# Kernel tuning notes

Measured on AMD Instinct MI355X. Metric: run time of the kernel, lower is better.

## Reference

```python
import jax, jax.numpy as jnp
import numpy as np

BATCH, IN_DIM, HID, OUT_DIM, Z = 8192, 2048, 4096, 2048, 4
CONN_P = 0.5  # Bernoulli keep-probability y


def random_activation(h, ids):
    # ids: [dim] int32 in [0,5); per-channel nonlinearity applied over batch.
    ids = ids[None, :]
    return jnp.select(
        [ids == 0, ids == 1, ids == 2, ids == 3],
        [jax.nn.relu(h), jax.nn.sigmoid(h), jnp.tanh(h), jnp.where(h >= 0, h, 0.1 * h)],
        jax.nn.selu(h),
    )


def _make_linear(key, fan_in, fan_out):
    kw, kb, km = jax.random.split(key, 3)
    w = jax.random.normal(kw, (fan_out, fan_in), dtype=jnp.float32)
    mask = jax.random.bernoulli(km, CONN_P, (fan_out, fan_in)).astype(jnp.float32)
    b = jax.random.normal(kb, (fan_out,), dtype=jnp.float32)
    return w * mask, b


def setup_inputs() -> dict:
    key = jax.random.key(0)
    ks = jax.random.split(key, 16)
    inp = {"input_pattern": jax.random.normal(ks[0], (BATCH, IN_DIM), dtype=jnp.float32)}
    dims = [(IN_DIM, HID)] + [(HID, HID)] * Z + [(HID, OUT_DIM)]  # z+2 Linear layers
    for i, (fi, fo) in enumerate(dims):
        w, b = _make_linear(ks[1 + i], fi, fo)
        inp[f"w{i}"] = w
        inp[f"b{i}"] = b
        inp[f"ids{i}"] = jax.random.randint(ks[8 + i], (fo,), 0, 5, dtype=jnp.int32)
    return inp


def reference(input_pattern, w0, b0, ids0, w1, b1, ids1, w2, b2, ids2,
              w3, b3, ids3, w4, b4, ids4, w5, b5, ids5):
    ws = (w0, w1, w2, w3, w4, w5)
    bs = (b0, b1, b2, b3, b4, b5)
    ids = (ids0, ids1, ids2, ids3, ids4, ids5)
    h = input_pattern
    for w, b, i in zip(ws, bs, ids):
        h = random_activation(h @ w.T + b, i)
    return h
```

## Files before the change

### kernel.cpp

```cpp
#include <hip/hip_runtime.h>

typedef _Float16 f16;
typedef _Float16 f16x8 __attribute__((ext_vector_type(8)));
typedef float f32x4 __attribute__((ext_vector_type(4)));

__device__ __forceinline__ void gload_lds16(const void* g, void* l) {
  __builtin_amdgcn_global_load_lds(
      (const __attribute__((address_space(1))) void*)g,
      (__attribute__((address_space(3))) void*)l, 16, 0, 0);
}

__device__ __forceinline__ float act_apply(float x, int id) {
  switch (id) {
    case 0: return fmaxf(x, 0.0f);
    case 1: return 1.0f / (1.0f + __expf(-x));
    case 2: return tanhf(x);
    case 3: return x >= 0.0f ? x : 0.1f * x;
    default: return 1.0507009873554805f *
                    (x > 0.0f ? x : 1.6732632423543772f * expm1f(x));
  }
}

__global__ __launch_bounds__(256, 3)
void gemm128w(const f16* __restrict__ A, const f16* __restrict__ W,
              const float* __restrict__ bias, const int* __restrict__ ids,
              float Sa, float invSn, f16* __restrict__ outp,
              int M, int N, int K) {
  __shared__ f16 LB[16384];
  const int tid  = (int)threadIdx.x;
  const int lane = tid & 63;
  const int wid  = tid >> 6;
  const int wr   = (wid >> 1) * 64;
  const int wc   = (wid & 1) * 64;

  const int nbc = N >> 7;
  const int b   = (int)blockIdx.x;
  const int x   = b & 7;
  const int r   = b >> 3;
  int brow, bcol;
  if (nbc >= 32) {
    brow = ((x >> 1) * 16 + (r & 15)) << 7;
    bcol = ((x & 1) * (nbc >> 1) + (r >> 4)) << 7;
  } else {
    brow = (x * 8 + (r & 7)) << 7;
    bcol = (r >> 3) << 7;
  }

  const int d0 = tid << 4;
  const int d1 = d0 + 4096;
  const int s0 = d0 ^ (((d0 >> 7) & 7) << 4);
  const int s1 = d1 ^ (((d1 >> 7) & 7) << 4);
  const int r0 = s0 >> 6, c0 = (s0 >> 4) & 3;
  const int r1 = s1 >> 6, c1 = (s1 >> 4) & 3;

  const f16* pA0 = A + (long)(brow + r0) * K + c0 * 8;
  const f16* pA1 = A + (long)(brow + r1) * K + c1 * 8;
  const int e0 = tid << 3;
  const int e1 = e0 + 2048;

  const int fr = lane & 15;
  const int kb = lane >> 4;
  const int xorv = ((fr >> 1) & 7) << 4;
  int offA[4];
#pragma unroll
  for (int m = 0; m < 4; ++m)
    offA[m] = (((wr + m * 16 + fr) << 6) + (kb << 4)) ^ xorv;

  const f16* pw[4];
#pragma unroll
  for (int n = 0; n < 4; ++n)
    pw[n] = W + (long)(bcol + wc + n * 16 + fr) * K + kb * 8;

  f32x4 acc[4][4];
#pragma unroll
  for (int m = 0; m < 4; ++m)
#pragma unroll
    for (int n = 0; n < 4; ++n) acc[m][n] = (f32x4){0.f, 0.f, 0.f, 0.f};

  const int nt = K >> 5;

  gload_lds16(pA0, &LB[e0]);
  gload_lds16(pA1, &LB[e1]);
  f16x8 w0[4], w1[4], af[4];
#pragma unroll
  for (int n = 0; n < 4; ++n) w0[n] = *(const f16x8*)(pw[n]);
  __syncthreads();

  for (int t = 0; t < nt; t += 2) {
    {
      const long kk = (long)(t + 1) << 5;
      gload_lds16(pA0 + kk, &LB[4096 + e0]);
      gload_lds16(pA1 + kk, &LB[4096 + e1]);
#pragma unroll
      for (int n = 0; n < 4; ++n) w1[n] = *(const f16x8*)(pw[n] + kk);
      const char* bA = (const char*)&LB[0];
#pragma unroll
      for (int m = 0; m < 4; ++m) af[m] = *(const f16x8*)(bA + offA[m]);
#pragma unroll
      for (int m = 0; m < 4; ++m)
#pragma unroll
        for (int n = 0; n < 4; ++n)
          acc[m][n] = __builtin_amdgcn_mfma_f32_16x16x32_f16(af[m], w0[n],
                                                             acc[m][n], 0, 0, 0);
      __syncthreads();
    }
    {
      if (t + 2 < nt) {
        const long kk = (long)(t + 2) << 5;
        gload_lds16(pA0 + kk, &LB[e0]);
        gload_lds16(pA1 + kk, &LB[e1]);
#pragma unroll
        for (int n = 0; n < 4; ++n) w0[n] = *(const f16x8*)(pw[n] + kk);
      }
      const char* bA = (const char*)&LB[0] + 8192;
#pragma unroll
      for (int m = 0; m < 4; ++m) af[m] = *(const f16x8*)(bA + offA[m]);
#pragma unroll
      for (int m = 0; m < 4; ++m)
#pragma unroll
        for (int n = 0; n < 4; ++n)
          acc[m][n] = __builtin_amdgcn_mfma_f32_16x16x32_f16(af[m], w1[n],
                                                             acc[m][n], 0, 0, 0);
      if (t + 2 < nt) __syncthreads();
    }
  }

  __syncthreads();
  char* eb = (char*)&LB[0] + wid * 8192;
  const int r4 = (lane >> 4) << 2;
#pragma unroll
  for (int n = 0; n < 4; ++n) {
    const int gcol = bcol + wc + n * 16 + fr;
    const float bv = bias[gcol];
    const int id   = ids[gcol];
#pragma unroll
    for (int m = 0; m < 4; ++m)
#pragma unroll
      for (int i = 0; i < 4; ++i) {
        const float y = act_apply(acc[m][n][i] * Sa + bv, id);
        const int w = ((m * 16 + r4 + i) * 64 + n * 16 + fr) * 2;
        *(f16*)(eb + (w ^ (((w >> 7) & 7) << 4))) = (f16)(y * invSn);
      }
  }
  __syncthreads();
#pragma unroll
  for (int j = 0; j < 8; ++j) {
    const int lrow = j * 8 + (lane >> 3);
    const int rd = lrow * 128 + (lane & 7) * 16;
    const f16x8 v = *(const f16x8*)(eb + (rd ^ (((rd >> 7) & 7) << 4)));
    *(f16x8*)&outp[(long)(brow + wr + lrow) * N + bcol + wc + (lane & 7) * 8] = v;
  }
}

template <bool FINAL>
__global__ __launch_bounds__(256, 4)
void gemm128(const f16* __restrict__ A, const f16* __restrict__ W,
             const float* __restrict__ bias, const int* __restrict__ ids,
             float Sa, float invSn, void* __restrict__ outv,
             int M, int N, int K) {
  __shared__ f16 lA[2][128 * 32];
  __shared__ f16 lB[2][128 * 32];

  const int tid  = (int)threadIdx.x;
  const int lane = tid & 63;
  const int wid  = tid >> 6;
  const int wr   = (wid >> 1) * 64;
  const int wc   = (wid & 1) * 64;

  const int nbc = N >> 7;
  const int b   = (int)blockIdx.x;
  const int x   = b & 7;
  const int r   = b >> 3;
  int brow, bcol;
  if (nbc >= 32) {
    brow = ((x >> 1) * 16 + (r & 15)) << 7;
    bcol = ((x & 1) * (nbc >> 1) + (r >> 4)) << 7;
  } else {
    brow = (x * 8 + (r & 7)) << 7;
    bcol = (r >> 3) << 7;
  }

  const int d0 = tid << 4;
  const int d1 = d0 + 4096;
  const int s0 = d0 ^ (((d0 >> 7) & 7) << 4);
  const int s1 = d1 ^ (((d1 >> 7) & 7) << 4);
  const int r0 = s0 >> 6, c0 = (s0 >> 4) & 3;
  const int r1 = s1 >> 6, c1 = (s1 >> 4) & 3;

  const f16* pA0 = A + (long)(brow + r0) * K + c0 * 8;
  const f16* pA1 = A + (long)(brow + r1) * K + c1 * 8;
  const f16* pB0 = W + (long)(bcol + r0) * K + c0 * 8;
  const f16* pB1 = W + (long)(bcol + r1) * K + c1 * 8;
  const int e0 = tid << 3;
  const int e1 = e0 + 2048;

  const int fr = lane & 15;
  const int kb = lane >> 4;
  const int xorv = ((fr >> 1) & 7) << 4;

  int offA[4], offB[4];
#pragma unroll
  for (int m = 0; m < 4; ++m)
    offA[m] = (((wr + m * 16 + fr) << 6) + (kb << 4)) ^ xorv;
#pragma unroll
  for (int n = 0; n < 4; ++n)
    offB[n] = (((wc + n * 16 + fr) << 6) + (kb << 4)) ^ xorv;

  f32x4 acc[4][4];
#pragma unroll
  for (int m = 0; m < 4; ++m)
#pragma unroll
    for (int n = 0; n < 4; ++n) acc[m][n] = (f32x4){0.f, 0.f, 0.f, 0.f};

  const int nt = K >> 5;
  int buf = 0;

  gload_lds16(pA0, &lA[0][e0]);
  gload_lds16(pA1, &lA[0][e1]);
  gload_lds16(pB0, &lB[0][e0]);
  gload_lds16(pB1, &lB[0][e1]);
  __syncthreads();

  for (int t = 0; t < nt; ++t) {
    if (t + 1 < nt) {
      const long kk = (long)(t + 1) << 5;
      gload_lds16(pA0 + kk, &lA[buf ^ 1][e0]);
      gload_lds16(pA1 + kk, &lA[buf ^ 1][e1]);
      gload_lds16(pB0 + kk, &lB[buf ^ 1][e0]);
      gload_lds16(pB1 + kk, &lB[buf ^ 1][e1]);
    }
    const char* bA = (const char*)&lA[buf][0];
    const char* bB = (const char*)&lB[buf][0];
    f16x8 af[4], bf[4];
#pragma unroll
    for (int m = 0; m < 4; ++m) af[m] = *(const f16x8*)(bA + offA[m]);
#pragma unroll
    for (int n = 0; n < 4; ++n) bf[n] = *(const f16x8*)(bB + offB[n]);
#pragma unroll
    for (int m = 0; m < 4; ++m)
#pragma unroll
      for (int n = 0; n < 4; ++n)
        acc[m][n] = __builtin_amdgcn_mfma_f32_16x16x32_f16(af[m], bf[n],
                                                           acc[m][n], 0, 0, 0);
    if (t + 1 < nt) {
      __syncthreads();
      buf ^= 1;
    }
  }

  const int r4 = (lane >> 4) << 2;
  if (!FINAL) {
    __syncthreads();
    char* eb = (char*)((wid < 2) ? &lA[wid][0] : &lB[wid - 2][0]);
#pragma unroll
    for (int n = 0; n < 4; ++n) {
      const int gcol = bcol + wc + n * 16 + fr;
      const float bv = bias[gcol];
      const int id   = ids[gcol];
#pragma unroll
      for (int m = 0; m < 4; ++m)
#pragma unroll
        for (int i = 0; i < 4; ++i) {
          const float y = act_apply(acc[m][n][i] * Sa + bv, id);
          const int w = ((m * 16 + r4 + i) * 64 + n * 16 + fr) * 2;
          *(f16*)(eb + (w ^ (((w >> 7) & 7) << 4))) = (f16)(y * invSn);
        }
    }
    __syncthreads();
    f16* outp = (f16*)outv;
#pragma unroll
    for (int j = 0; j < 8; ++j) {
      const int lrow = j * 8 + (lane >> 3);
      const int rd = lrow * 128 + (lane & 7) * 16;
      const f16x8 v = *(const f16x8*)(eb + (rd ^ (((rd >> 7) & 7) << 4)));
      *(f16x8*)&outp[(long)(brow + wr + lrow) * N + bcol + wc + (lane & 7) * 8] = v;
    }
  } else {
#pragma unroll
    for (int n = 0; n < 4; ++n) {
      const int gcol = bcol + wc + n * 16 + fr;
      const float bv = bias[gcol];
      const int id   = ids[gcol];
#pragma unroll
      for (int m = 0; m < 4; ++m) {
        const int grow = brow + wr + m * 16 + r4;
#pragma unroll
        for (int i = 0; i < 4; ++i) {
          const float y = act_apply(acc[m][n][i] * Sa + bv, id);
          ((float*)outv)[(long)(grow + i) * N + gcol] = y;
        }
      }
    }
  }
}

__global__ void cvt_f32_to_f16(const float* __restrict__ in, f16* __restrict__ out,
                               float scale, int n) {
  int i = ((int)blockIdx.x * 256 + (int)threadIdx.x) * 8;
  const int stride = (int)gridDim.x * 256 * 8;
  for (; i < n; i += stride) {
    const float4 v0 = *(const float4*)(in + i);
    const float4 v1 = *(const float4*)(in + i + 4);
    f16x8 h;
    h[0] = (f16)(v0.x * scale); h[1] = (f16)(v0.y * scale);
    h[2] = (f16)(v0.z * scale); h[3] = (f16)(v0.w * scale);
    h[4] = (f16)(v1.x * scale); h[5] = (f16)(v1.y * scale);
    h[6] = (f16)(v1.z * scale); h[7] = (f16)(v1.w * scale);
    *(f16x8*)(out + i) = h;
  }
}

extern "C" void kernel_launch(void* const* d_in, const int* in_sizes, int n_in,
                              void* d_out, int out_size, void* d_ws, size_t ws_size,
                              hipStream_t stream) {
  (void)in_sizes; (void)n_in; (void)out_size; (void)ws_size;
  const int M = 8192, IND = 2048, HID = 4096, OUTD = 2048;
  const float* x = (const float*)d_in[0];

  f16* actA = (f16*)d_ws;
  f16* actB = actA + (size_t)M * HID;
  f16* wbuf = actB + (size_t)M * HID;

  const float S[6] = {1.f, 16.f, 512.f, 16384.f, 262144.f, 8388608.f};
  const int Ks[6] = {IND, HID, HID, HID, HID, HID};
  const int Ns[6] = {HID, HID, HID, HID, HID, OUTD};

  cvt_f32_to_f16<<<2048, 256, 0, stream>>>(x, actA, 1.0f, M * IND);

  f16* cur = actA;
  f16* nxt = actB;
  for (int i = 0; i < 6; ++i) {
    const int K = Ks[i], N = Ns[i];
    const float* w  = (const float*)d_in[1 + 3 * i];
    const float* bs = (const float*)d_in[2 + 3 * i];
    const int* id   = (const int*)d_in[3 + 3 * i];

    cvt_f32_to_f16<<<2048, 256, 0, stream>>>(w, wbuf, 1.0f, N * K);

    const int nblk = (M >> 7) * (N >> 7);
    if (i == 1 || i == 2) {
      gemm128w<<<nblk, 256, 0, stream>>>(
          cur, wbuf, bs, id, S[i], 1.0f / S[i + 1], nxt, M, N, K);
      f16* t = cur; cur = nxt; nxt = t;
    } else if (i < 5) {
      gemm128<false><<<nblk, 256, 0, stream>>>(
          cur, wbuf, bs, id, S[i], 1.0f / S[i + 1], nxt, M, N, K);
      f16* t = cur; cur = nxt; nxt = t;
    } else {
      gemm128<true><<<nblk, 256, 0, stream>>>(
          cur, wbuf, bs, id, S[i], 1.0f, d_out, M, N, K);
    }
  }
}
```

Measured before the change: 2.398 ms.

## Stage weights through LDS with triple-buffered pipeline in layer 1-2 GEMM

The GEMM used for layers 1 and 2 no longer loads weight fragments straight from global memory into registers. Both A and B tiles now go into LDS through a 3-slot ring filled by direct global-to-LDS loads issued two steps ahead. Each k-step takes one explicit vmcnt wait and one barrier instead of a double-buffered pair of syncs. LDS use grows from 32KB to 48KB per block, which may limit the 3-blocks-per-CU occupancy target, and the epilogue reuses the A ring (24KB) as scratch, which looks smaller than the 32KB the four waves write.

```diff
diff --git a/kernel.cpp b/kernel.cpp
--- a/kernel.cpp
+++ b/kernel.cpp
@@ -22,11 +22,13 @@
 }
 
 __global__ __launch_bounds__(256, 3)
-void gemm128w(const f16* __restrict__ A, const f16* __restrict__ W,
+void gemm128r(const f16* __restrict__ A, const f16* __restrict__ W,
               const float* __restrict__ bias, const int* __restrict__ ids,
               float Sa, float invSn, f16* __restrict__ outp,
               int M, int N, int K) {
-  __shared__ f16 LB[16384];
+  __shared__ f16 rA[3][4096];
+  __shared__ f16 rB[3][4096];
+
   const int tid  = (int)threadIdx.x;
   const int lane = tid & 63;
   const int wid  = tid >> 6;
@@ -55,21 +57,22 @@
 
   const f16* pA0 = A + (long)(brow + r0) * K + c0 * 8;
   const f16* pA1 = A + (long)(brow + r1) * K + c1 * 8;
+  const f16* pB0 = W + (long)(bcol + r0) * K + c0 * 8;
+  const f16* pB1 = W + (long)(bcol + r1) * K + c1 * 8;
   const int e0 = tid << 3;
   const int e1 = e0 + 2048;
 
   const int fr = lane & 15;
   const int kb = lane >> 4;
   const int xorv = ((fr >> 1) & 7) << 4;
-  int offA[4];
+
+  int offA[4], offB[4];
 #pragma unroll
   for (int m = 0; m < 4; ++m)
     offA[m] = (((wr + m * 16 + fr) << 6) + (kb << 4)) ^ xorv;
-
-  const f16* pw[4];
 #pragma unroll
   for (int n = 0; n < 4; ++n)
-    pw[n] = W + (long)(bcol + wc + n * 16 + fr) * K + kb * 8;
+    offB[n] = (((wc + n * 16 + fr) << 6) + (kb << 4)) ^ xorv;
 
   f32x4 acc[4][4];
 #pragma unroll
@@ -79,54 +82,50 @@
 
   const int nt = K >> 5;
 
-  gload_lds16(pA0, &LB[e0]);
-  gload_lds16(pA1, &LB[e1]);
-  f16x8 w0[4], w1[4], af[4];
-#pragma unroll
-  for (int n = 0; n < 4; ++n) w0[n] = *(const f16x8*)(pw[n]);
+#define RSTAGE(T)                               \
+  do {                                          \
+    const int _sl = (T) % 3;                    \
+    const long _k = (long)(T) << 5;             \
+    gload_lds16(pA0 + _k, &rA[_sl][e0]);        \
+    gload_lds16(pA1 + _k, &rA[_sl][e1]);        \
+    gload_lds16(pB0 + _k, &rB[_sl][e0]);        \
+    gload_lds16(pB1 + _k, &rB[_sl][e1]);        \
+  } while (0)
+
+  RSTAGE(0);
+  RSTAGE(1);
+  asm volatile("s_waitcnt vmcnt(4)" ::: "memory");
+  __builtin_amdgcn_s_barrier();
+  asm volatile("" ::: "memory");
+
+  for (int t = 0; t < nt; ++t) {
+    if (t + 2 < nt) RSTAGE(t + 2);
+
+    const int sl = t % 3;
+    const char* bA = (const char*)&rA[sl][0];
+    const char* bB = (const char*)&rB[sl][0];
+    f16x8 af[4], bf[4];
+#pragma unroll
+    for (int m = 0; m < 4; ++m) af[m] = *(const f16x8*)(bA + offA[m]);
+#pragma unroll
+    for (int n = 0; n < 4; ++n) bf[n] = *(const f16x8*)(bB + offB[n]);
+#pragma unroll
+    for (int m = 0; m < 4; ++m)
+#pragma unroll
+      for (int n = 0; n < 4; ++n)
+        acc[m][n] = __builtin_amdgcn_mfma_f32_16x16x32_f16(af[m], bf[n],
+                                                           acc[m][n], 0, 0, 0);
+    if (t + 1 < nt) {
+      if (t + 2 < nt) asm volatile("s_waitcnt vmcnt(4)" ::: "memory");
+      else            asm volatile("s_waitcnt vmcnt(0)" ::: "memory");
+      __builtin_amdgcn_s_barrier();
+      asm volatile("" ::: "memory");
+    }
+  }
+#undef RSTAGE
+
   __syncthreads();
-
-  for (int t = 0; t < nt; t += 2) {
-    {
-      const long kk = (long)(t + 1) << 5;
-      gload_lds16(pA0 + kk, &LB[4096 + e0]);
-      gload_lds16(pA1 + kk, &LB[4096 + e1]);
-#pragma unroll
-      for (int n = 0; n < 4; ++n) w1[n] = *(const f16x8*)(pw[n] + kk);
-      const char* bA = (const char*)&LB[0];
-#pragma unroll
-      for (int m = 0; m < 4; ++m) af[m] = *(const f16x8*)(bA + offA[m]);
-#pragma unroll
-      for (int m = 0; m < 4; ++m)
-#pragma unroll
-        for (int n = 0; n < 4; ++n)
-          acc[m][n] = __builtin_amdgcn_mfma_f32_16x16x32_f16(af[m], w0[n],
-                                                             acc[m][n], 0, 0, 0);
-      __syncthreads();
-    }
-    {
-      if (t + 2 < nt) {
-        const long kk = (long)(t + 2) << 5;
-        gload_lds16(pA0 + kk, &LB[e0]);
-        gload_lds16(pA1 + kk, &LB[e1]);
-#pragma unroll
-        for (int n = 0; n < 4; ++n) w0[n] = *(const f16x8*)(pw[n] + kk);
-      }
-      const char* bA = (const char*)&LB[0] + 8192;
-#pragma unroll
-      for (int m = 0; m < 4; ++m) af[m] = *(const f16x8*)(bA + offA[m]);
-#pragma unroll
-      for (int m = 0; m < 4; ++m)
-#pragma unroll
-        for (int n = 0; n < 4; ++n)
-          acc[m][n] = __builtin_amdgcn_mfma_f32_16x16x32_f16(af[m], w1[n],
-                                                             acc[m][n], 0, 0, 0);
-      if (t + 2 < nt) __syncthreads();
-    }
-  }
-
-  __syncthreads();
-  char* eb = (char*)&LB[0] + wid * 8192;
+  char* eb = (char*)&rA[0][0] + wid * 8192;
   const int r4 = (lane >> 4) << 2;
 #pragma unroll
   for (int n = 0; n < 4; ++n) {
@@ -339,7 +338,7 @@
 
     const int nblk = (M >> 7) * (N >> 7);
     if (i == 1 || i == 2) {
-      gemm128w<<<nblk, 256, 0, stream>>>(
+      gemm128r<<<nblk, 256, 0, stream>>>(
           cur, wbuf, bs, id, S[i], 1.0f / S[i + 1], nxt, M, N, K);
       f16* t = cur; cur = nxt; nxt = t;
     } else if (i < 5) {
```

After: 2.003 ms. 1.2x faster.
